# Performance work log

Hardware: AMD Instinct MI355X
Metric: run time of the kernel (lower is better)

The kernel has to match this reference:

```python
import jax, jax.numpy as jnp
import numpy as np

B, N, CZ, CH, CA, H, TN = 1, 256, 128, 128, 32, 4, 4


def setup_inputs() -> dict:
    key = jax.random.key(0)
    ks = iter(jax.random.split(key, 64))

    def rn(shape, s=0.02):
        return jax.random.normal(next(ks), shape, dtype=jnp.float32) * s

    d = {"z": jax.random.normal(next(ks), (B, N, N, CZ), dtype=jnp.float32)}
    # Triangle multiplication params, stacked [2, ...]: idx 0 = outgoing, 1 = incoming
    d["tm_ln_in_w"] = jnp.ones((2, CZ)); d["tm_ln_in_b"] = jnp.zeros((2, CZ))
    for nm, shp in [("ap", (2, CZ, CH)), ("ag", (2, CZ, CH)), ("bp", (2, CZ, CH)),
                    ("bg", (2, CZ, CH)), ("g", (2, CZ, CZ)), ("zo", (2, CH, CZ))]:
        d[f"tm_{nm}_w"] = rn(shp)
        d[f"tm_{nm}_b"] = jnp.zeros((2, shp[-1]))
    d["tm_lnout_w"] = jnp.ones((2, CH)); d["tm_lnout_b"] = jnp.zeros((2, CH))
    # Triangle attention params, stacked [2, ...]: idx 0 = start, 1 = end
    d["ta_ln_w"] = jnp.ones((2, CZ)); d["ta_ln_b"] = jnp.zeros((2, CZ))
    d["ta_q_w"] = rn((2, CZ, H * CA)); d["ta_k_w"] = rn((2, CZ, H * CA)); d["ta_v_w"] = rn((2, CZ, H * CA))
    d["ta_b_w"] = rn((2, CZ, H))
    d["ta_g_w"] = rn((2, CZ, H * CA)); d["ta_g_b"] = jnp.zeros((2, H * CA))
    d["ta_o_w"] = rn((2, H * CA, CZ)); d["ta_o_b"] = jnp.zeros((2, CZ))
    # Pair transition
    d["pt_ln_w"] = jnp.ones((CZ,)); d["pt_ln_b"] = jnp.zeros((CZ,))
    d["pt_1_w"] = rn((CZ, TN * CZ)); d["pt_1_b"] = jnp.zeros((TN * CZ,))
    d["pt_2_w"] = rn((TN * CZ, CZ)); d["pt_2_b"] = jnp.zeros((CZ,))
    return d


def _ln(x, w, b, eps=1e-5):
    m = jnp.mean(x, axis=-1, keepdims=True)
    v = jnp.mean(jnp.square(x - m), axis=-1, keepdims=True)
    return (x - m) * jax.lax.rsqrt(v + eps) * w + b


def _tri_mul(z, lnw, lnb, apw, apb, agw, agb, bpw, bpb, bgw, bgb, gw, gb,
             lnow, lnob, zw, zb, outgoing):
    x = _ln(z, lnw, lnb)
    a = jax.nn.sigmoid(x @ agw + agb) * (x @ apw + apb)  # [B,I,J,CH]
    b = jax.nn.sigmoid(x @ bgw + bgb) * (x @ bpw + bpb)
    eq = 'bikc,bjkc->bijc' if outgoing else 'bkic,bkjc->bijc'
    t = jnp.einsum(eq, a, b)  # O(N^3 * CH)
    t = _ln(t, lnow, lnob) @ zw + zb
    return t * jax.nn.sigmoid(x @ gw + gb)


def _tri_att(z, lnw, lnb, qw, kw, vw, bw, gw, gb, ow, ob):
    Bz, I, J, _ = z.shape
    x = _ln(z, lnw, lnb)
    # triangle bias [B,1,H,I,J] (broadcast over query row)
    bias = jnp.einsum('bijc,ch->bhij', x, bw)[:, None]
    q = (x @ qw).reshape(Bz, I, J, H, CA).transpose(0, 1, 3, 2, 4) / np.float32(np.sqrt(CA))
    k = (x @ kw).reshape(Bz, I, J, H, CA).transpose(0, 1, 3, 2, 4)
    v = (x @ vw).reshape(Bz, I, J, H, CA).transpose(0, 1, 3, 2, 4)
    a = jnp.einsum('bihqc,bihkc->bihqk', q, k) + bias  # [B,I,H,J,J]
    p = jax.nn.softmax(a, axis=-1)
    o = jnp.einsum('bihqk,bihkc->bihqc', p, v).transpose(0, 1, 3, 2, 4).reshape(Bz, I, J, H * CA)
    o = o * jax.nn.sigmoid(x @ gw + gb)
    return o @ ow + ob


def reference(z, tm_ln_in_w, tm_ln_in_b, tm_ap_w, tm_ap_b, tm_ag_w, tm_ag_b,
              tm_bp_w, tm_bp_b, tm_bg_w, tm_bg_b, tm_g_w, tm_g_b,
              tm_lnout_w, tm_lnout_b, tm_zo_w, tm_zo_b,
              ta_ln_w, ta_ln_b, ta_q_w, ta_k_w, ta_v_w, ta_b_w,
              ta_g_w, ta_g_b, ta_o_w, ta_o_b,
              pt_ln_w, pt_ln_b, pt_1_w, pt_1_b, pt_2_w, pt_2_b):
    def tm(zz, i, outgoing):
        return _tri_mul(zz, tm_ln_in_w[i], tm_ln_in_b[i], tm_ap_w[i], tm_ap_b[i],
                        tm_ag_w[i], tm_ag_b[i], tm_bp_w[i], tm_bp_b[i],
                        tm_bg_w[i], tm_bg_b[i], tm_g_w[i], tm_g_b[i],
                        tm_lnout_w[i], tm_lnout_b[i], tm_zo_w[i], tm_zo_b[i], outgoing)

    def ta(zz, i):
        return _tri_att(zz, ta_ln_w[i], ta_ln_b[i], ta_q_w[i], ta_k_w[i], ta_v_w[i],
                        ta_b_w[i], ta_g_w[i], ta_g_b[i], ta_o_w[i], ta_o_b[i])

    z = z + tm(z, 0, True)          # triangle mult outgoing + residual (dropout = eval identity)
    z = z + tm(z, 1, False)         # triangle mult incoming + residual
    z = z + ta(z, 0)                # triangle attention (starting node)
    zt = jnp.swapaxes(z, 1, 2)      # transpose for ending-node attention
    zt = zt + ta(zt, 1)
    z = jnp.swapaxes(zt, 1, 2)
    x = _ln(z, pt_ln_w, pt_ln_b)    # pair transition
    z = z + (jax.nn.relu(x @ pt_1_w + pt_1_b) @ pt_2_w + pt_2_b)
    return z
```

## Files before the change

### kernel.cpp

```cpp
#include <hip/hip_runtime.h>
#include <math.h>

#define N_  256
#define NN  65536
#define CZ  128
#define CH  128
#define H_  4
#define CA  32

typedef __attribute__((ext_vector_type(8))) short bf16x8;
typedef __attribute__((ext_vector_type(4))) float f32x4;

__device__ __forceinline__ float sigmoidf_(float x){ return 1.f/(1.f+__expf(-x)); }

__device__ __forceinline__ short f2b(float f){
  unsigned u = __float_as_uint(f);
  unsigned r = (u + 0x7fffu + ((u>>16)&1u)) >> 16;
  return (short)r;
}
__device__ __forceinline__ float b2f(short s){
  unsigned u = ((unsigned)(unsigned short)s) << 16;
  return __uint_as_float(u);
}
__device__ __forceinline__ unsigned pk_bf16(float lo, float hi){
  unsigned r;
  asm volatile("v_cvt_pk_bf16_f32 %0, %1, %2" : "=v"(r) : "v"(lo), "v"(hi));
  return r;
}

__device__ __forceinline__ void glds16(const void* g, const void* l){
  __builtin_amdgcn_global_load_lds((const __attribute__((address_space(1))) void*)g,
                                   (__attribute__((address_space(3))) void*)l, 16, 0, 0);
}

__device__ __forceinline__ float wave_red_sum(float v){
  #pragma unroll
  for(int o=32;o>0;o>>=1) v += __shfl_xor(v,o,64);
  return v;
}

__device__ __forceinline__ int Gperm(int t, int m){
  return ((t>>1)<<5) + ((m>>2)<<3) + ((t&1)<<2) + (m&3);
}

__global__ void __launch_bounds__(256) prep_weights(
    const float* tm_ag, const float* tm_ap, const float* tm_bg, const float* tm_bp,
    const float* tm_g, const float* tm_zo,
    const float* ta_q, const float* ta_k, const float* ta_v, const float* ta_g, const float* ta_o,
    const float* pt1, const float* pt2, short* Wf){
  int tid = threadIdx.x;
  int g = blockIdx.x*4 + (tid>>6);
  int l = tid & 63;
  int s = blockIdx.y;
  const float* src; int ldn = 128, koff = 0, noff = 0;
  if (s < 12){
    int i = s/6, w = s - i*6;
    switch(w){ case 0: src=tm_ag; break; case 1: src=tm_ap; break; case 2: src=tm_bg; break;
               case 3: src=tm_bp; break; case 4: src=tm_g;  break; default: src=tm_zo; }
    src += i*16384;
  } else if (s < 22){
    int t2 = s-12; int i = t2/5, w = t2 - i*5;
    switch(w){ case 0: src=ta_q; break; case 1: src=ta_k; break; case 2: src=ta_v; break;
               case 3: src=ta_g; break; default: src=ta_o; }
    src += i*16384;
  } else if (s < 26){
    src = pt1; ldn = 512; noff = (s-22)*128;
  } else {
    src = pt2; koff = (s-26)*128;
  }
  int nt = g>>2, ks = g&3;
  int n = noff + nt*16 + (l&15);
  int kb = koff + ks*32 + (l>>4)*8;
  short tmp[8];
  #pragma unroll
  for (int e=0;e<8;e++) tmp[e] = f2b(src[(size_t)(kb+e)*ldn + n]);
  short* dst = Wf + s*16384 + ((nt*4+ks)*64 + l)*8;
  *(short4*)dst     = *(short4*)&tmp[0];
  *(short4*)(dst+4) = *(short4*)&tmp[4];
}

template<bool TRANS>
__global__ void __launch_bounds__(256) ln_x(const float* __restrict__ in,
                                            const float* __restrict__ w,
                                            const float* __restrict__ b,
                                            short* __restrict__ out){
  int wid  = threadIdx.x >> 6;
  int lane = threadIdx.x & 63;
  int row  = blockIdx.x*4 + wid;
  int irow;
  if (TRANS){ int i = row >> 8, j = row & 255; irow = (j<<8) | i; } else irow = row;
  float v0 = in[(size_t)irow*CZ + lane];
  float v1 = in[(size_t)irow*CZ + lane + 64];
  float m  = wave_red_sum(v0+v1) * (1.f/128.f);
  float d0 = v0-m, d1 = v1-m;
  float var = wave_red_sum(d0*d0 + d1*d1) * (1.f/128.f);
  float r = rsqrtf(var + 1e-5f);
  out[(size_t)row*CZ + lane]      = f2b(d0*r*w[lane]    + b[lane]);
  out[(size_t)row*CZ + lane + 64] = f2b(d1*r*w[lane+64] + b[lane+64]);
}

__device__ __forceinline__ void stage128_8(const short* __restrict__ g, short* xs, int r0, int tid){
  #pragma unroll
  for (int m=0;m<4;++m){
    int d = m*512 + tid;
    int row = d>>4, cw = d&15;
    glds16(&g[(size_t)(r0+row)*128 + ((cw ^ (row&15))<<3)], xs + (size_t)(d & ~63)*8);
  }
}

__device__ __forceinline__ bf16x8 ldsA(const short* xs, int row, int ch){
  return *(const bf16x8*)&xs[row*128 + ((ch ^ (row&15))<<3)];
}

__device__ __forceinline__ void stageW(const short* __restrict__ wf, int h, short* wb, int tid){
  #pragma unroll
  for (int r=0;r<2;++r){
    int s = r*512 + tid;
    int ch = s>>6, ln = s&63;
    glds16(wf + (size_t)(((ch>>1)*4 + h*2 + (ch&1))*64 + ln)*8, wb + (size_t)(s & ~63)*8);
  }
}

__device__ __forceinline__ void core_half(const short* xs, const short* wb, int h,
                                          int wm, int wn, int l, f32x4 (&acc)[2][4]){
  #pragma unroll
  for (int ks2=0; ks2<2; ++ks2){
    bf16x8 a[2], b[4];
    #pragma unroll
    for (int mt=0; mt<2; ++mt)
      a[mt] = ldsA(xs, wm*32 + mt*16 + (l&15), (h*2+ks2)*4 + (l>>4));
    #pragma unroll
    for (int nt=0; nt<4; ++nt)
      b[nt] = *(const bf16x8*)&wb[(size_t)(((wn*4+nt)*2 + ks2)*64 + l)*8];
    #pragma unroll
    for (int mt=0; mt<2; ++mt)
      #pragma unroll
      for (int nt=0; nt<4; ++nt)
        acc[mt][nt] = __builtin_amdgcn_mfma_f32_16x16x32_bf16(a[mt], b[nt], acc[mt][nt], 0,0,0);
  }
}

#define ZERO_ACC(A) { _Pragma("unroll") for(int _a=0;_a<2;_a++) _Pragma("unroll") for(int _b=0;_b<4;_b++) A[_a][_b]=(f32x4){0,0,0,0}; }

#define GEMM_PROLOG8 \
  int tid = threadIdx.x; int r0 = blockIdx.x*128; \
  int wid = tid>>6, l = tid&63; int wm = wid>>1, wn = wid&1; (void)r0;

#define EPI8 \
  int row = wm*32 + mt*16 + ((l>>4)<<2) + reg; \
  int col = wn*64 + nt*16 + (l&15);

#define FOR_EPI for (int mt=0;mt<2;++mt) for (int nt=0;nt<4;++nt) for (int reg=0;reg<4;++reg)

#define SCATTER_PACKED(P, LDSBUF) \
  _Pragma("unroll") \
  for (int mt=0;mt<2;++mt) \
    _Pragma("unroll") \
    for (int nt=0;nt<4;++nt){ \
      int row0 = wm*32 + mt*16 + ((l>>4)<<2); \
      int col  = wn*64 + nt*16 + (l&15); \
      unsigned lo = (unsigned)P[mt][nt].x, hi = (unsigned)P[mt][nt].y; \
      LDSBUF[(row0  )*128 + (((col>>3) ^ ((row0  )&15))<<3) + (col&7)] = (short)(lo & 0xffff); \
      LDSBUF[(row0+1)*128 + (((col>>3) ^ ((row0+1)&15))<<3) + (col&7)] = (short)(lo >> 16); \
      LDSBUF[(row0+2)*128 + (((col>>3) ^ ((row0+2)&15))<<3) + (col&7)] = (short)(hi & 0xffff); \
      LDSBUF[(row0+3)*128 + (((col>>3) ^ ((row0+3)&15))<<3) + (col&7)] = (short)(hi >> 16); \
    }

#define STORE_TILE(OUT, LDSBUF) \
  _Pragma("unroll") \
  for (int m2=0;m2<4;++m2){ \
    int d = m2*512 + tid; int row = d>>4, ch = d&15; \
    *(int4*)&OUT[(size_t)(r0+row)*128 + ch*8] = *(const int4*)&LDSBUF[row*128 + ((ch ^ (row&15))<<3)]; \
  }

__global__ void __launch_bounds__(512,4) k_quad_gate(const short* __restrict__ X,
                                                     const short* __restrict__ Wagf, const float* __restrict__ bag,
                                                     const short* __restrict__ Wapf, const float* __restrict__ bap,
                                                     const short* __restrict__ Wbgf, const float* __restrict__ bbg,
                                                     const short* __restrict__ Wbpf, const float* __restrict__ bbp,
                                                     short* __restrict__ out1, short* __restrict__ out2){
  __shared__ short xs[16384];
  __shared__ short wb[2][8192];
  short* wbf = &wb[0][0];
  GEMM_PROLOG8
  stageW(Wagf, 0, wb[0], tid);
  stage128_8(X, xs, r0, tid);
  __syncthreads();
  int2 o1[2][4], o2[2][4];
  {
    f32x4 ag[2][4], ap[2][4];
    ZERO_ACC(ag) ZERO_ACC(ap)
    stageW(Wagf, 1, wb[1], tid); core_half(xs, wb[0], 0, wm, wn, l, ag); __syncthreads();
    stageW(Wapf, 0, wb[0], tid); core_half(xs, wb[1], 1, wm, wn, l, ag); __syncthreads();
    stageW(Wapf, 1, wb[1], tid); core_half(xs, wb[0], 0, wm, wn, l, ap); __syncthreads();
    stageW(Wbgf, 0, wb[0], tid); core_half(xs, wb[1], 1, wm, wn, l, ap); __syncthreads();
    #pragma unroll
    for (int mt=0;mt<2;++mt)
      #pragma unroll
      for (int nt=0;nt<4;++nt){
        int col = wn*64 + nt*16 + (l&15);
        float bgc = bag[col], bpc = bap[col];
        float v0 = (ap[mt][nt][0]+bpc)*sigmoidf_(ag[mt][nt][0]+bgc);
        float v1 = (ap[mt][nt][1]+bpc)*sigmoidf_(ag[mt][nt][1]+bgc);
        float v2 = (ap[mt][nt][2]+bpc)*sigmoidf_(ag[mt][nt][2]+bgc);
        float v3 = (ap[mt][nt][3]+bpc)*sigmoidf_(ag[mt][nt][3]+bgc);
        o1[mt][nt].x = (int)pk_bf16(v0,v1);
        o1[mt][nt].y = (int)pk_bf16(v2,v3);
      }
  }
  {
    f32x4 bg2[2][4], bp2[2][4];
    ZERO_ACC(bg2) ZERO_ACC(bp2)
    stageW(Wbgf, 1, wb[1], tid); core_half(xs, wb[0], 0, wm, wn, l, bg2); __syncthreads();
    stageW(Wbpf, 0, wb[0], tid); core_half(xs, wb[1], 1, wm, wn, l, bg2); __syncthreads();
    stageW(Wbpf, 1, wb[1], tid); core_half(xs, wb[0], 0, wm, wn, l, bp2); __syncthreads();
    core_half(xs, wb[1], 1, wm, wn, l, bp2);
    #pragma unroll
    for (int mt=0;mt<2;++mt)
      #pragma unroll
      for (int nt=0;nt<4;++nt){
        int col = wn*64 + nt*16 + (l&15);
        float bgc = bbg[col], bpc = bbp[col];
        float v0 = (bp2[mt][nt][0]+bpc)*sigmoidf_(bg2[mt][nt][0]+bgc);
        float v1 = (bp2[mt][nt][1]+bpc)*sigmoidf_(bg2[mt][nt][1]+bgc);
        float v2 = (bp2[mt][nt][2]+bpc)*sigmoidf_(bg2[mt][nt][2]+bgc);
        float v3 = (bp2[mt][nt][3]+bpc)*sigmoidf_(bg2[mt][nt][3]+bgc);
        o2[mt][nt].x = (int)pk_bf16(v0,v1);
        o2[mt][nt].y = (int)pk_bf16(v2,v3);
      }
  }
  __syncthreads();
  SCATTER_PACKED(o1, wbf)
  __syncthreads();
  STORE_TILE(out1, wbf)
  __syncthreads();
  SCATTER_PACKED(o2, wbf)
  __syncthreads();
  STORE_TILE(out2, wbf)
}

__global__ void __launch_bounds__(512,4) k_qkv(const short* __restrict__ X,
                                               const short* __restrict__ Wqf, float sq,
                                               const short* __restrict__ Wkf,
                                               const short* __restrict__ Wvf,
                                               const float* __restrict__ bw,
                                               short* __restrict__ out_q, short* __restrict__ out_k,
                                               short* __restrict__ Vt, float* __restrict__ BSF){
  __shared__ short xs[16384];
  __shared__ short wb[2][8192];
  short* wbf = &wb[0][0];
  GEMM_PROLOG8
  stageW(Wqf, 0, wb[0], tid);
  stage128_8(X, xs, r0, tid);
  __syncthreads();
  int2 oq[2][4], ok[2][4];
  {
    f32x4 aq[2][4], ak[2][4];
    ZERO_ACC(aq) ZERO_ACC(ak)
    stageW(Wqf, 1, wb[1], tid); core_half(xs, wb[0], 0, wm, wn, l, aq); __syncthreads();
    stageW(Wkf, 0, wb[0], tid); core_half(xs, wb[1], 1, wm, wn, l, aq); __syncthreads();
    #pragma unroll
    for (int mt=0;mt<2;++mt)
      #pragma unroll
      for (int nt=0;nt<4;++nt){
        oq[mt][nt].x = (int)pk_bf16(aq[mt][nt][0]*sq, aq[mt][nt][1]*sq);
        oq[mt][nt].y = (int)pk_bf16(aq[mt][nt][2]*sq, aq[mt][nt][3]*sq);
      }
    stageW(Wkf, 1, wb[1], tid); core_half(xs, wb[0], 0, wm, wn, l, ak); __syncthreads();
    stageW(Wvf, 0, wb[0], tid); core_half(xs, wb[1], 1, wm, wn, l, ak); __syncthreads();
    #pragma unroll
    for (int mt=0;mt<2;++mt)
      #pragma unroll
      for (int nt=0;nt<4;++nt){
        ok[mt][nt].x = (int)pk_bf16(ak[mt][nt][0], ak[mt][nt][1]);
        ok[mt][nt].y = (int)pk_bf16(ak[mt][nt][2], ak[mt][nt][3]);
      }
  }
  f32x4 av[2][4];
  ZERO_ACC(av)
  stageW(Wvf, 1, wb[1], tid); core_half(xs, wb[0], 0, wm, wn, l, av); __syncthreads();
  core_half(xs, wb[1], 1, wm, wn, l, av);
  {
    int rl = tid & 127, hh = tid >> 7;
    float bacc = 0.f;
    #pragma unroll
    for (int ch=0; ch<16; ++ch){
      bf16x8 v = ldsA(xs, rl, ch);
      #pragma unroll
      for (int e=0;e<8;++e) bacc += b2f(v[e]) * bw[(ch*8+e)*H_ + hh];
    }
    int r = r0 + rl;
    int qq = r >> 8, j = r & 255;
    int t = ((j>>5)<<1) + ((j>>2)&1);
    int mm = (((j>>3)&3)<<2) + (j&3);
    int idx = (((hh*16 + (qq>>4))*16 + t) << 8) + (((mm>>2)*16 + (qq&15)) << 2) + (mm&3);
    BSF[idx] = bacc;
  }
  __syncthreads();
  #pragma unroll
  for (int mt=0;mt<2;++mt)
    #pragma unroll
    for (int nt=0;nt<4;++nt){
      int rb  = wm*32 + mt*16 + ((l>>4)<<2);
      int col = wn*64 + nt*16 + (l&15);
      short4 s4 = { f2b(av[mt][nt][0]), f2b(av[mt][nt][1]), f2b(av[mt][nt][2]), f2b(av[mt][nt][3]) };
      *(short4*)&xs[col*128 + (((rb>>3) ^ (col&15))<<3) + (rb&7)] = s4;
    }
  __syncthreads();
  int i = r0>>8, j0 = r0&255;
  #pragma unroll
  for (int m=0;m<4;++m){
    int d = m*512 + tid;
    int c = d>>4, ch = d&15;
    int4 val = *(const int4*)&xs[c*128 + ((ch ^ (c&15))<<3)];
    *(int4*)&Vt[(size_t)((i*4 + (c>>5))*32 + (c&31))*256 + j0 + ch*8] = val;
  }
  SCATTER_PACKED(oq, wbf)
  __syncthreads();
  STORE_TILE(out_q, wbf)
  __syncthreads();
  SCATTER_PACKED(ok, wbf)
  __syncthreads();
  STORE_TILE(out_k, wbf)
}

__global__ void __launch_bounds__(512,2) k_tri_finish(const short* __restrict__ Tb,
                                                      const short* __restrict__ X,
                                                      const short* __restrict__ Wzf, const float* __restrict__ bz,
                                                      const short* __restrict__ Wgf, const float* __restrict__ bg,
                                                      const float* __restrict__ lnw, const float* __restrict__ lnb,
                                                      const float* __restrict__ zin, float* __restrict__ zout){
  __shared__ short tt[16384];
  __shared__ short xs[16384];
  __shared__ short wb[2][8192];
  __shared__ float ps[512], pq[512];
  __shared__ float mu[128], iv[128];
  GEMM_PROLOG8
  stageW(Wzf, 0, wb[0], tid);
  stage128_8(X, xs, r0, tid);
  #pragma unroll
  for (int m=0;m<4;++m){
    int d = m*512 + tid;
    int c = d>>4, ch = d&15;
    glds16(&Tb[(size_t)c*65536 + r0 + ch*8], tt + (size_t)(d & ~63)*8);
  }
  __syncthreads();
  int rl = tid & 127, cq = tid >> 7;
  float vals[32]; float s = 0.f, q = 0.f;
  #pragma unroll
  for (int cc=0; cc<32; ++cc){
    float v = b2f(tt[(cq*32+cc)*128 + rl]);
    vals[cc] = v; s += v; q += v*v;
  }
  ps[cq*128 + rl] = s; pq[cq*128 + rl] = q;
  __syncthreads();
  if (tid < 128){
    float ss = ps[tid]+ps[128+tid]+ps[256+tid]+ps[384+tid];
    float qq = pq[tid]+pq[128+tid]+pq[256+tid]+pq[384+tid];
    float m = ss * (1.f/128.f);
    float var = qq * (1.f/128.f) - m*m;
    mu[tid] = m; iv[tid] = rsqrtf(var + 1e-5f);
  }
  __syncthreads();
  {
    float m = mu[rl], r = iv[rl];
    #pragma unroll
    for (int chq=0; chq<4; ++chq){
      short tmp[8];
      #pragma unroll
      for (int e=0;e<8;++e){
        int cc = chq*8 + e;
        int c = cq*32 + cc;
        tmp[e] = f2b((vals[cc]-m)*r*lnw[c] + lnb[c]);
      }
      int ch = cq*4 + chq;
      *(int4*)&tt[rl*128 + ((ch ^ (rl&15))<<3)] = *(int4*)tmp;
    }
  }
  __syncthreads();
  f32x4 az[2][4], ag[2][4];
  ZERO_ACC(az) ZERO_ACC(ag)
  stageW(Wzf, 1, wb[1], tid); core_half(tt, wb[0], 0, wm, wn, l, az); __syncthreads();
  stageW(Wgf, 0, wb[0], tid); core_half(tt, wb[1], 1, wm, wn, l, az); __syncthreads();
  stageW(Wgf, 1, wb[1], tid); core_half(xs, wb[0], 0, wm, wn, l, ag); __syncthreads();
  core_half(xs, wb[1], 1, wm, wn, l, ag);
  FOR_EPI{
    EPI8
    size_t idx = (size_t)(r0+row)*128 + col;
    float v = (az[mt][nt][reg] + bz[col]) * sigmoidf_(ag[mt][nt][reg] + bg[col]);
    zout[idx] = zin[idx] + v;
  }
}

template<bool TRANS>
__global__ void __launch_bounds__(512,2) k_attn_out(const short* __restrict__ O,
                                                    const short* __restrict__ X,
                                                    const short* __restrict__ Wgf, const float* __restrict__ bg,
                                                    const short* __restrict__ Wof, const float* __restrict__ bo,
                                                    float* __restrict__ z){
  __shared__ short xs[16384];
  __shared__ short os[16384];
  __shared__ short wb[2][8192];
  GEMM_PROLOG8
  stageW(Wgf, 0, wb[0], tid);
  stage128_8(X, xs, r0, tid);
  #pragma unroll
  for (int m=0;m<4;++m){
    int d = m*512 + tid;
    int row = d>>4, ch = d&15;
    glds16(&O[(size_t)(r0+row)*128 + ch*8], os + (size_t)(d & ~63)*8);
  }
  __syncthreads();
  f32x4 ag[2][4];
  ZERO_ACC(ag)
  stageW(Wgf, 1, wb[1], tid); core_half(xs, wb[0], 0, wm, wn, l, ag); __syncthreads();
  stageW(Wof, 0, wb[0], tid); core_half(xs, wb[1], 1, wm, wn, l, ag); __syncthreads();
  stageW(Wof, 1, wb[1], tid);
  FOR_EPI{
    EPI8
    float ov = b2f(os[row*128 + col]);
    float v = ov * sigmoidf_(ag[mt][nt][reg] + bg[col]);
    xs[row*128 + (((col>>3) ^ (row&15))<<3) + (col&7)] = f2b(v);
  }
  __syncthreads();
  f32x4 a2[2][4];
  ZERO_ACC(a2)
  core_half(xs, wb[0], 0, wm, wn, l, a2);
  core_half(xs, wb[1], 1, wm, wn, l, a2);
  FOR_EPI{
    EPI8
    int orow = r0+row;
    int zrow = TRANS ? (((orow&255)<<8) | (orow>>8)) : orow;
    z[(size_t)zrow*128 + col] += a2[mt][nt][reg] + bo[col];
  }
}

__global__ void __launch_bounds__(512,2) k_pt(const float* __restrict__ lnw, const float* __restrict__ lnb,
                                              const short* __restrict__ W1f, const float* __restrict__ b1,
                                              const short* __restrict__ W2f, const float* __restrict__ b2,
                                              float* __restrict__ z){
  __shared__ short xs[16384];
  __shared__ short hs[16384];
  __shared__ short wb[2][8192];
  __shared__ float ps[512], pq[512];
  __shared__ float mu[128], iv[128];
  GEMM_PROLOG8
  stageW(W1f, 0, wb[0], tid);
  int rl = tid & 127, cq = tid >> 7;
  float vals[32]; float s = 0.f, q = 0.f;
  {
    const float* zr = &z[(size_t)(r0+rl)*128 + cq*32];
    #pragma unroll
    for (int cc=0; cc<32; cc+=4){
      float4 v4 = *(const float4*)&zr[cc];
      vals[cc]=v4.x; vals[cc+1]=v4.y; vals[cc+2]=v4.z; vals[cc+3]=v4.w;
      s += v4.x+v4.y+v4.z+v4.w;
      q += v4.x*v4.x + v4.y*v4.y + v4.z*v4.z + v4.w*v4.w;
    }
  }
  ps[cq*128 + rl] = s; pq[cq*128 + rl] = q;
  __syncthreads();
  if (tid < 128){
    float ss = ps[tid]+ps[128+tid]+ps[256+tid]+ps[384+tid];
    float qq = pq[tid]+pq[128+tid]+pq[256+tid]+pq[384+tid];
    float m = ss * (1.f/128.f);
    float var = qq * (1.f/128.f) - m*m;
    mu[tid] = m; iv[tid] = rsqrtf(var + 1e-5f);
  }
  __syncthreads();
  {
    float m = mu[rl], r = iv[rl];
    #pragma unroll
    for (int chq=0; chq<4; ++chq){
      short tmp[8];
      #pragma unroll
      for (int e=0;e<8;++e){
        int cc = chq*8 + e;
        int c = cq*32 + cc;
        tmp[e] = f2b((vals[cc]-m)*r*lnw[c] + lnb[c]);
      }
      int ch = cq*4 + chq;
      *(int4*)&xs[rl*128 + ((ch ^ (rl&15))<<3)] = *(int4*)tmp;
    }
  }
  __syncthreads();
  f32x4 a2[2][4];
  ZERO_ACC(a2)
  for (int m=0;m<4;++m){
    f32x4 a1[2][4];
    ZERO_ACC(a1)
    stageW(W1f + m*16384, 1, wb[1], tid); core_half(xs, wb[0], 0, wm, wn, l, a1); __syncthreads();
    stageW(W2f + m*16384, 0, wb[0], tid); core_half(xs, wb[1], 1, wm, wn, l, a1); __syncthreads();
    stageW(W2f + m*16384, 1, wb[1], tid);
    FOR_EPI{
      EPI8
      float v = fmaxf(a1[mt][nt][reg] + b1[m*128 + col], 0.f);
      hs[row*128 + (((col>>3) ^ (row&15))<<3) + (col&7)] = f2b(v);
    }
    __syncthreads();
    core_half(hs, wb[0], 0, wm, wn, l, a2);
    __syncthreads();
    if (m<3) stageW(W1f + (m+1)*16384, 0, wb[0], tid);
    core_half(hs, wb[1], 1, wm, wn, l, a2);
    __syncthreads();
  }
  FOR_EPI{
    EPI8
    z[(size_t)(r0+row)*128 + col] += a2[mt][nt][reg] + b2[col];
  }
}

template<bool TR>
__global__ void __launch_bounds__(256) pack_cxy(const short* __restrict__ inA, const short* __restrict__ inB,
                                                short* __restrict__ outA, short* __restrict__ outB){
  __shared__ short tile[256*144];
  const short* in = blockIdx.y ? inB : inA;
  short* out      = blockIdx.y ? outB : outA;
  int x = blockIdx.x, tid = threadIdx.x;
  #pragma unroll
  for (int m=0;m<16;++m){
    int idx = m*256 + tid;
    int y = idx>>4, c0 = (idx&15)*8;
    int r = TR ? (y*256 + x) : (x*256 + y);
    *(int4*)&tile[y*144 + c0] = *(const int4*)&in[(size_t)r*128 + c0];
  }
  __syncthreads();
  int c = tid & 127, yh = tid >> 7;
  short* ob = out + (size_t)c*65536 + x*256 + yh*128;
  #pragma unroll
  for (int yc=0; yc<16; ++yc){
    short tmp[8];
    #pragma unroll
    for (int e=0;e<8;e++) tmp[e] = tile[(yh*128 + yc*8 + e)*144 + c];
    *(int4*)&ob[yc*8] = *(int4*)tmp;
  }
}

__global__ void __launch_bounds__(512,4) k_einsum(const short* __restrict__ Ab,
                                                  const short* __restrict__ Bb,
                                                  short* __restrict__ Tb){
  __shared__ short as[2][128*64];
  __shared__ short bs[2][128*64];
  int c = blockIdx.z;
  int i0 = blockIdx.x*128, j0 = blockIdx.y*128;
  const short* A = Ab + (size_t)c*65536;
  const short* B = Bb + (size_t)c*65536;
  int tid = threadIdx.x;
  int wid = tid>>6, l = tid&63; int wm = wid>>1, wn = wid&1;
  f32x4 acc[2][4];
  ZERO_ACC(acc)

  #define ESTAGE(buf, kt) { \
    _Pragma("unroll") \
    for (int m_=0;m_<2;++m_){ \
      int d_ = m_*512 + tid; \
      int row_ = d_>>3, cw_ = d_&7; \
      glds16(&A[(size_t)(i0+row_)*256 + (kt)*64 + ((cw_ ^ (row_&7))<<3)], &as[buf][(d_ & ~63)*8]); \
      glds16(&B[(size_t)(j0+row_)*256 + (kt)*64 + ((cw_ ^ (row_&7))<<3)], &bs[buf][(d_ & ~63)*8]); \
    } }

  ESTAGE(0, 0)
  __syncthreads();
  for (int kt=0; kt<4; ++kt){
    int cur = kt & 1;
    if (kt < 3) ESTAGE(cur^1, kt+1)
    #pragma unroll
    for (int ks=0; ks<2; ++ks){
// ... 83 lines not shown
      w4.x = pk_bf16(acc[2*jt  ][0], acc[2*jt  ][1]);
      w4.y = pk_bf16(acc[2*jt  ][2], acc[2*jt  ][3]);
      w4.z = pk_bf16(acc[2*jt+1][0], acc[2*jt+1][1]);
      w4.w = pk_bf16(acc[2*jt+1][2], acc[2*jt+1][3]);
      pf[jt] = *(bf16x8*)&w4;
    }
    #pragma unroll
    for (int ct=0; ct<2; ++ct){
      f32x4 oe = {0.f,0.f,0.f,0.f}, oo = {0.f,0.f,0.f,0.f};
      #pragma unroll
      for (int jt=0;jt<8;jt+=2){
        bf16x8 ve = *(const bf16x8*)&Vf[((ct*8 + jt  )*64 + l)*8];
        bf16x8 vo = *(const bf16x8*)&Vf[((ct*8 + jt+1)*64 + l)*8];
        oe = __builtin_amdgcn_mfma_f32_16x16x32_bf16(ve, pf[jt  ], oe, 0,0,0);
        oo = __builtin_amdgcn_mfma_f32_16x16x32_bf16(vo, pf[jt+1], oo, 0,0,0);
      }
      int q = sub*16 + ln;
      int c = ct*16 + lg*4;
      short4 ov = { f2b((oe[0]+oo[0])*iv), f2b((oe[1]+oo[1])*iv),
                    f2b((oe[2]+oo[2])*iv), f2b((oe[3]+oo[3])*iv) };
      *(short4*)&O[(size_t)(i*N_ + q)*CH + h*CA + c] = ov;
    }
  }
}

extern "C" void kernel_launch(void* const* d_in, const int* in_sizes, int n_in,
                              void* d_out, int out_size, void* d_ws, size_t ws_size,
                              hipStream_t stream) {
  const float* z_in      = (const float*)d_in[0];
  const float* tm_lnin_w = (const float*)d_in[1];
  const float* tm_lnin_b = (const float*)d_in[2];
  const float* tm_ap_w   = (const float*)d_in[3];
  const float* tm_ap_b   = (const float*)d_in[4];
  const float* tm_ag_w   = (const float*)d_in[5];
  const float* tm_ag_b   = (const float*)d_in[6];
  const float* tm_bp_w   = (const float*)d_in[7];
  const float* tm_bp_b   = (const float*)d_in[8];
  const float* tm_bg_w   = (const float*)d_in[9];
  const float* tm_bg_b   = (const float*)d_in[10];
  const float* tm_g_w    = (const float*)d_in[11];
  const float* tm_g_b    = (const float*)d_in[12];
  const float* tm_zo_w   = (const float*)d_in[13];
  const float* tm_zo_b   = (const float*)d_in[14];
  const float* tm_lno_w  = (const float*)d_in[15];
  const float* tm_lno_b  = (const float*)d_in[16];
  const float* ta_ln_w   = (const float*)d_in[17];
  const float* ta_ln_b   = (const float*)d_in[18];
  const float* ta_q_w    = (const float*)d_in[19];
  const float* ta_k_w    = (const float*)d_in[20];
  const float* ta_v_w    = (const float*)d_in[21];
  const float* ta_b_w    = (const float*)d_in[22];
  const float* ta_g_w    = (const float*)d_in[23];
  const float* ta_g_b    = (const float*)d_in[24];
  const float* ta_o_w    = (const float*)d_in[25];
  const float* ta_o_b    = (const float*)d_in[26];
  const float* pt_ln_w   = (const float*)d_in[27];
  const float* pt_ln_b   = (const float*)d_in[28];
  const float* pt_1_w    = (const float*)d_in[29];
  const float* pt_1_b    = (const float*)d_in[30];
  const float* pt_2_w    = (const float*)d_in[31];
  const float* pt_2_b    = (const float*)d_in[32];

  float* z  = (float*)d_out;
  char* base = (char*)d_ws;
  const size_t MB = 1u<<20;
  short* wf  = (short*)base;
  short* Xb  = (short*)(base + 1*MB);
  short* R1  = (short*)(base + 17*MB);
  short* R2  = (short*)(base + 33*MB);
  short* R3  = (short*)(base + 49*MB);
  short* R4  = (short*)(base + 65*MB);
  short* Tb  = (short*)(base + 81*MB);
  float* BSF = (float*)(base + 113*MB);

  #define SL(s) (wf + (size_t)(s)*16384)

  prep_weights<<<dim3(8,30), 256, 0, stream>>>(tm_ag_w, tm_ap_w, tm_bg_w, tm_bp_w,
                                               tm_g_w, tm_zo_w,
                                               ta_q_w, ta_k_w, ta_v_w, ta_g_w, ta_o_w,
                                               pt_1_w, pt_2_w, wf);

  for (int i=0;i<2;i++){
    const float* zsrc = (i==0) ? z_in : z;
    ln_x<false><<<NN/4, 256, 0, stream>>>(zsrc, tm_lnin_w+i*CZ, tm_lnin_b+i*CZ, Xb);
    k_quad_gate<<<NN/128, 512, 0, stream>>>(Xb, SL(i*6+0), tm_ag_b+i*CH, SL(i*6+1), tm_ap_b+i*CH,
                                            SL(i*6+2), tm_bg_b+i*CH, SL(i*6+3), tm_bp_b+i*CH,
                                            R1, R2);
    if (i==0) pack_cxy<false><<<dim3(256,2), 256, 0, stream>>>(R1, R2, R3, R4);
    else      pack_cxy<true ><<<dim3(256,2), 256, 0, stream>>>(R1, R2, R3, R4);
    k_einsum<<<dim3(2,2,128), 512, 0, stream>>>(R3, R4, Tb);
    k_tri_finish<<<NN/128, 512, 0, stream>>>(Tb, Xb, SL(i*6+5), tm_zo_b+i*CZ,
                                             SL(i*6+4), tm_g_b+i*CZ,
                                             tm_lno_w+i*CH, tm_lno_b+i*CH, zsrc, z);
  }

  for (int i=0;i<2;i++){
    if (i==0) ln_x<false><<<NN/4, 256, 0, stream>>>(z, ta_ln_w, ta_ln_b, Xb);
    else      ln_x<true ><<<NN/4, 256, 0, stream>>>(z, ta_ln_w+CZ, ta_ln_b+CZ, Xb);
    k_qkv<<<NN/128, 512, 0, stream>>>(Xb, SL(12+i*5+0), 0.17677669529663687f,
                                      SL(12+i*5+1), SL(12+i*5+2), ta_b_w+i*CZ*H_,
                                      R1, R2, R3, BSF);
    attn_mfma<<<dim3(N_,H_), 256, 0, stream>>>(R1, R2, R3, BSF, R4);
    if (i==0) k_attn_out<false><<<NN/128, 512, 0, stream>>>(R4, Xb, SL(12+i*5+3), ta_g_b+i*H_*CA,
                                                            SL(12+i*5+4), ta_o_b+i*CZ, z);
    else      k_attn_out<true ><<<NN/128, 512, 0, stream>>>(R4, Xb, SL(12+i*5+3), ta_g_b+i*H_*CA,
                                                            SL(12+i*5+4), ta_o_b+i*CZ, z);
  }

  k_pt<<<NN/128, 512, 0, stream>>>(pt_ln_w, pt_ln_b, SL(22), pt_1_b, SL(26), pt_2_b, z);
}
```

Before: 534.9 us.

## Fuse input layernorm into projection GEMMs and shrink row tiles to 64

Removes the standalone ln_x kernels by computing the layernorm inside k_gg and k_qkv, which write the normalized bf16 tile to Xb for later consumers. All row-tiled GEMM kernels go from 128-row/512-thread blocks to 64-row/256-thread blocks, doubling the grid and cutting LDS per block. This saves a separate launch and one fp32 read pass per layernorm. In exchange, weight tiles are staged twice as often relative to the work done, and the extra Xb store adds to the fused kernels.

Measured after the change: 516.1 us. 3.5% less time.

```diff
diff --git a/kernel.cpp b/kernel.cpp
--- a/kernel.cpp
+++ b/kernel.cpp
@@ -31,12 +31,6 @@
 __device__ __forceinline__ void glds16(const void* g, const void* l){
   __builtin_amdgcn_global_load_lds((const __attribute__((address_space(1))) void*)g,
                                    (__attribute__((address_space(3))) void*)l, 16, 0, 0);
-}
-
-__device__ __forceinline__ float wave_red_sum(float v){
-  #pragma unroll
-  for(int o=32;o>0;o>>=1) v += __shfl_xor(v,o,64);
-  return v;
 }
 
 __device__ __forceinline__ int Gperm(int t, int m){
@@ -79,30 +73,10 @@
   *(short4*)(dst+4) = *(short4*)&tmp[4];
 }
 
-template<bool TRANS>
-__global__ void __launch_bounds__(256) ln_x(const float* __restrict__ in,
-                                            const float* __restrict__ w,
-                                            const float* __restrict__ b,
-                                            short* __restrict__ out){
-  int wid  = threadIdx.x >> 6;
-  int lane = threadIdx.x & 63;
-  int row  = blockIdx.x*4 + wid;
-  int irow;
-  if (TRANS){ int i = row >> 8, j = row & 255; irow = (j<<8) | i; } else irow = row;
-  float v0 = in[(size_t)irow*CZ + lane];
-  float v1 = in[(size_t)irow*CZ + lane + 64];
-  float m  = wave_red_sum(v0+v1) * (1.f/128.f);
-  float d0 = v0-m, d1 = v1-m;
-  float var = wave_red_sum(d0*d0 + d1*d1) * (1.f/128.f);
-  float r = rsqrtf(var + 1e-5f);
-  out[(size_t)row*CZ + lane]      = f2b(d0*r*w[lane]    + b[lane]);
-  out[(size_t)row*CZ + lane + 64] = f2b(d1*r*w[lane+64] + b[lane+64]);
-}
-
-__device__ __forceinline__ void stage128_8(const short* __restrict__ g, short* xs, int r0, int tid){
+__device__ __forceinline__ void stage64(const short* __restrict__ g, short* xs, int r0, int tid){
   #pragma unroll
   for (int m=0;m<4;++m){
-    int d = m*512 + tid;
+    int d = m*256 + tid;
     int row = d>>4, cw = d&15;
     glds16(&g[(size_t)(r0+row)*128 + ((cw ^ (row&15))<<3)], xs + (size_t)(d & ~63)*8);
   }
@@ -114,8 +88,8 @@
 
 __device__ __forceinline__ void stageW(const short* __restrict__ wf, int h, short* wb, int tid){
   #pragma unroll
-  for (int r=0;r<2;++r){
-    int s = r*512 + tid;
+  for (int r=0;r<4;++r){
+    int s = r*256 + tid;
     int ch = s>>6, ln = s&63;
     glds16(wf + (size_t)(((ch>>1)*4 + h*2 + (ch&1))*64 + ln)*8, wb + (size_t)(s & ~63)*8);
   }
@@ -142,8 +116,8 @@
 
 #define ZERO_ACC(A) { _Pragma("unroll") for(int _a=0;_a<2;_a++) _Pragma("unroll") for(int _b=0;_b<4;_b++) A[_a][_b]=(f32x4){0,0,0,0}; }
 
-#define GEMM_PROLOG8 \
-  int tid = threadIdx.x; int r0 = blockIdx.x*128; \
+#define GEMM_PROLOG \
+  int tid = threadIdx.x; int r0 = blockIdx.x*64; \
   int wid = tid>>6, l = tid&63; int wm = wid>>1, wn = wid&1; (void)r0;
 
 #define EPI8 \
@@ -169,96 +143,141 @@
 #define STORE_TILE(OUT, LDSBUF) \
   _Pragma("unroll") \
   for (int m2=0;m2<4;++m2){ \
-    int d = m2*512 + tid; int row = d>>4, ch = d&15; \
+    int d = m2*256 + tid; int row = d>>4, ch = d&15; \
     *(int4*)&OUT[(size_t)(r0+row)*128 + ch*8] = *(const int4*)&LDSBUF[row*128 + ((ch ^ (row&15))<<3)]; \
   }
 
-__global__ void __launch_bounds__(512,4) k_quad_gate(const short* __restrict__ X,
-                                                     const short* __restrict__ Wagf, const float* __restrict__ bag,
-                                                     const short* __restrict__ Wapf, const float* __restrict__ bap,
-                                                     const short* __restrict__ Wbgf, const float* __restrict__ bbg,
-                                                     const short* __restrict__ Wbpf, const float* __restrict__ bbp,
-                                                     short* __restrict__ out1, short* __restrict__ out2){
-  __shared__ short xs[16384];
+template<bool TRANS>
+__device__ __forceinline__ void ln_prolog(const float* __restrict__ zsrc,
+                                          const float* __restrict__ lnw,
+                                          const float* __restrict__ lnb,
+                                          int r0, int tid, short* xs,
+                                          float* ps, float* pq, float* mu, float* iv){
+  int rl = tid & 63, cq = tid >> 6;
+  int r = r0 + rl;
+  int sr = TRANS ? (((r&255)<<8) | (r>>8)) : r;
+  float vals[32]; float s=0.f, q=0.f;
+  const float* zr = &zsrc[(size_t)sr*128 + cq*32];
+  #pragma unroll
+  for (int cc=0; cc<32; cc+=4){
+    float4 v4 = *(const float4*)&zr[cc];
+    vals[cc]=v4.x; vals[cc+1]=v4.y; vals[cc+2]=v4.z; vals[cc+3]=v4.w;
+    s += v4.x+v4.y+v4.z+v4.w;
+    q += v4.x*v4.x+v4.y*v4.y+v4.z*v4.z+v4.w*v4.w;
+  }
+  ps[cq*64+rl]=s; pq[cq*64+rl]=q;
+  __syncthreads();
+  if (tid < 64){
+    float ss = ps[tid]+ps[64+tid]+ps[128+tid]+ps[192+tid];
+    float qq = pq[tid]+pq[64+tid]+pq[128+tid]+pq[192+tid];
+    float m = ss*(1.f/128.f);
+    float var = qq*(1.f/128.f) - m*m;
+    mu[tid]=m; iv[tid]=rsqrtf(var+1e-5f);
+  }
+  __syncthreads();
+  float m = mu[rl], rv = iv[rl];
+  #pragma unroll
+  for (int chq=0; chq<4; ++chq){
+    short tmp[8];
+    #pragma unroll
+    for (int e=0;e<8;++e){
+      int cc = chq*8+e, c = cq*32+cc;
+      tmp[e] = f2b((vals[cc]-m)*rv*lnw[c] + lnb[c]);
+    }
+    int ch = cq*4 + chq;
+    *(int4*)&xs[rl*128 + ((ch ^ (rl&15))<<3)] = *(int4*)tmp;
+  }
+}
+
+__global__ void __launch_bounds__(256,4) k_gg(const float* __restrict__ zsrc,
+                                              const float* __restrict__ lnw, const float* __restrict__ lnb,
+                                              const short* __restrict__ Wagf, const float* __restrict__ bag,
+                                              const short* __restrict__ Wapf, const float* __restrict__ bap,
+                                              const short* __restrict__ Wbgf, const float* __restrict__ bbg,
+                                              const short* __restrict__ Wbpf, const float* __restrict__ bbp,
+                                              short* __restrict__ Xb,
+                                              short* __restrict__ out1, short* __restrict__ out2){
+  __shared__ short xs[8192];
   __shared__ short wb[2][8192];
-  short* wbf = &wb[0][0];
-  GEMM_PROLOG8
+  __shared__ float ps[256], pq[256], mu[64], iv[64];
+  GEMM_PROLOG
   stageW(Wagf, 0, wb[0], tid);
-  stage128_8(X, xs, r0, tid);
-  __syncthreads();
+  ln_prolog<false>(zsrc, lnw, lnb, r0, tid, xs, ps, pq, mu, iv);
+  __syncthreads();
+  STORE_TILE(Xb, xs)
   int2 o1[2][4], o2[2][4];
   {
-    f32x4 ag[2][4], ap[2][4];
-    ZERO_ACC(ag) ZERO_ACC(ap)
-    stageW(Wagf, 1, wb[1], tid); core_half(xs, wb[0], 0, wm, wn, l, ag); __syncthreads();
-    stageW(Wapf, 0, wb[0], tid); core_half(xs, wb[1], 1, wm, wn, l, ag); __syncthreads();
-    stageW(Wapf, 1, wb[1], tid); core_half(xs, wb[0], 0, wm, wn, l, ap); __syncthreads();
-    stageW(Wbgf, 0, wb[0], tid); core_half(xs, wb[1], 1, wm, wn, l, ap); __syncthreads();
+    f32x4 ag[2][4]; ZERO_ACC(ag)
+    stageW(Wagf,1,wb[1],tid); core_half(xs,wb[0],0,wm,wn,l,ag); __syncthreads();
+    stageW(Wapf,0,wb[0],tid); core_half(xs,wb[1],1,wm,wn,l,ag); __syncthreads();
+    f32x4 ap[2][4]; ZERO_ACC(ap)
+    stageW(Wapf,1,wb[1],tid); core_half(xs,wb[0],0,wm,wn,l,ap); __syncthreads();
+    stageW(Wbgf,0,wb[0],tid); core_half(xs,wb[1],1,wm,wn,l,ap); __syncthreads();
     #pragma unroll
     for (int mt=0;mt<2;++mt)
       #pragma unroll
       for (int nt=0;nt<4;++nt){
         int col = wn*64 + nt*16 + (l&15);
         float bgc = bag[col], bpc = bap[col];
-        float v0 = (ap[mt][nt][0]+bpc)*sigmoidf_(ag[mt][nt][0]+bgc);
-        float v1 = (ap[mt][nt][1]+bpc)*sigmoidf_(ag[mt][nt][1]+bgc);
-        float v2 = (ap[mt][nt][2]+bpc)*sigmoidf_(ag[mt][nt][2]+bgc);
-        float v3 = (ap[mt][nt][3]+bpc)*sigmoidf_(ag[mt][nt][3]+bgc);
-        o1[mt][nt].x = (int)pk_bf16(v0,v1);
-        o1[mt][nt].y = (int)pk_bf16(v2,v3);
+        o1[mt][nt].x = (int)pk_bf16((ap[mt][nt][0]+bpc)*sigmoidf_(ag[mt][nt][0]+bgc),
+                                    (ap[mt][nt][1]+bpc)*sigmoidf_(ag[mt][nt][1]+bgc));
+        o1[mt][nt].y = (int)pk_bf16((ap[mt][nt][2]+bpc)*sigmoidf_(ag[mt][nt][2]+bgc),
+                                    (ap[mt][nt][3]+bpc)*sigmoidf_(ag[mt][nt][3]+bgc));
       }
   }
   {
-    f32x4 bg2[2][4], bp2[2][4];
-    ZERO_ACC(bg2) ZERO_ACC(bp2)
-    stageW(Wbgf, 1, wb[1], tid); core_half(xs, wb[0], 0, wm, wn, l, bg2); __syncthreads();
-    stageW(Wbpf, 0, wb[0], tid); core_half(xs, wb[1], 1, wm, wn, l, bg2); __syncthreads();
-    stageW(Wbpf, 1, wb[1], tid); core_half(xs, wb[0], 0, wm, wn, l, bp2); __syncthreads();
-    core_half(xs, wb[1], 1, wm, wn, l, bp2);
+    f32x4 bg2[2][4]; ZERO_ACC(bg2)
+    stageW(Wbgf,1,wb[1],tid); core_half(xs,wb[0],0,wm,wn,l,bg2); __syncthreads();
+    stageW(Wbpf,0,wb[0],tid); core_half(xs,wb[1],1,wm,wn,l,bg2); __syncthreads();
+    f32x4 bp2[2][4]; ZERO_ACC(bp2)
+    stageW(Wbpf,1,wb[1],tid); core_half(xs,wb[0],0,wm,wn,l,bp2); __syncthreads();
+    core_half(xs,wb[1],1,wm,wn,l,bp2);
     #pragma unroll
     for (int mt=0;mt<2;++mt)
       #pragma unroll
       for (int nt=0;nt<4;++nt){
         int col = wn*64 + nt*16 + (l&15);
         float bgc = bbg[col], bpc = bbp[col];
-        float v0 = (bp2[mt][nt][0]+bpc)*sigmoidf_(bg2[mt][nt][0]+bgc);
-        float v1 = (bp2[mt][nt][1]+bpc)*sigmoidf_(bg2[mt][nt][1]+bgc);
-        float v2 = (bp2[mt][nt][2]+bpc)*sigmoidf_(bg2[mt][nt][2]+bgc);
-        float v3 = (bp2[mt][nt][3]+bpc)*sigmoidf_(bg2[mt][nt][3]+bgc);
-        o2[mt][nt].x = (int)pk_bf16(v0,v1);
-        o2[mt][nt].y = (int)pk_bf16(v2,v3);
+        o2[mt][nt].x = (int)pk_bf16((bp2[mt][nt][0]+bpc)*sigmoidf_(bg2[mt][nt][0]+bgc),
+                                    (bp2[mt][nt][1]+bpc)*sigmoidf_(bg2[mt][nt][1]+bgc));
+        o2[mt][nt].y = (int)pk_bf16((bp2[mt][nt][2]+bpc)*sigmoidf_(bg2[mt][nt][2]+bgc),
+                                    (bp2[mt][nt][3]+bpc)*sigmoidf_(bg2[mt][nt][3]+bgc));
       }
   }
   __syncthreads();
-  SCATTER_PACKED(o1, wbf)
-  __syncthreads();
-  STORE_TILE(out1, wbf)
-  __syncthreads();
-  SCATTER_PACKED(o2, wbf)
-  __syncthreads();
-  STORE_TILE(out2, wbf)
-}
-
-__global__ void __launch_bounds__(512,4) k_qkv(const short* __restrict__ X,
+  SCATTER_PACKED(o1, xs)
+  __syncthreads();
+  STORE_TILE(out1, xs)
+  __syncthreads();
+  SCATTER_PACKED(o2, xs)
+  __syncthreads();
+  STORE_TILE(out2, xs)
+}
+
+template<bool TRANS>
+__global__ void __launch_bounds__(256,4) k_qkv(const float* __restrict__ zsrc,
+                                               const float* __restrict__ lnw, const float* __restrict__ lnb,
                                                const short* __restrict__ Wqf, float sq,
                                                const short* __restrict__ Wkf,
                                                const short* __restrict__ Wvf,
                                                const float* __restrict__ bw,
+                                               short* __restrict__ Xb,
                                                short* __restrict__ out_q, short* __restrict__ out_k,
                                                short* __restrict__ Vt, float* __restrict__ BSF){
-  __shared__ short xs[16384];
+  __shared__ short xs[8192];
   __shared__ short wb[2][8192];
-  short* wbf = &wb[0][0];
-  GEMM_PROLOG8
+  __shared__ float ps[256], pq[256], mu[64], iv[64];
+  GEMM_PROLOG
   stageW(Wqf, 0, wb[0], tid);
-  stage128_8(X, xs, r0, tid);
-  __syncthreads();
+  ln_prolog<TRANS>(zsrc, lnw, lnb, r0, tid, xs, ps, pq, mu, iv);
+  __syncthreads();
+  STORE_TILE(Xb, xs)
   int2 oq[2][4], ok[2][4];
+  f32x4 av[2][4];
   {
-    f32x4 aq[2][4], ak[2][4];
-    ZERO_ACC(aq) ZERO_ACC(ak)
-    stageW(Wqf, 1, wb[1], tid); core_half(xs, wb[0], 0, wm, wn, l, aq); __syncthreads();
-    stageW(Wkf, 0, wb[0], tid); core_half(xs, wb[1], 1, wm, wn, l, aq); __syncthreads();
+    f32x4 aq[2][4]; ZERO_ACC(aq)
+    stageW(Wqf,1,wb[1],tid); core_half(xs,wb[0],0,wm,wn,l,aq); __syncthreads();
+    stageW(Wkf,0,wb[0],tid); core_half(xs,wb[1],1,wm,wn,l,aq); __syncthreads();
     #pragma unroll
     for (int mt=0;mt<2;++mt)
       #pragma unroll
@@ -266,8 +285,11 @@
         oq[mt][nt].x = (int)pk_bf16(aq[mt][nt][0]*sq, aq[mt][nt][1]*sq);
         oq[mt][nt].y = (int)pk_bf16(aq[mt][nt][2]*sq, aq[mt][nt][3]*sq);
       }
-    stageW(Wkf, 1, wb[1], tid); core_half(xs, wb[0], 0, wm, wn, l, ak); __syncthreads();
-    stageW(Wvf, 0, wb[0], tid); core_half(xs, wb[1], 1, wm, wn, l, ak); __syncthreads();
+  }
+  {
+    f32x4 ak[2][4]; ZERO_ACC(ak)
+    stageW(Wkf,1,wb[1],tid); core_half(xs,wb[0],0,wm,wn,l,ak); __syncthreads();
+    stageW(Wvf,0,wb[0],tid); core_half(xs,wb[1],1,wm,wn,l,ak); __syncthreads();
     #pragma unroll
     for (int mt=0;mt<2;++mt)
       #pragma unroll
@@ -276,12 +298,11 @@
         ok[mt][nt].y = (int)pk_bf16(ak[mt][nt][2], ak[mt][nt][3]);
       }
   }
-  f32x4 av[2][4];
   ZERO_ACC(av)
-  stageW(Wvf, 1, wb[1], tid); core_half(xs, wb[0], 0, wm, wn, l, av); __syncthreads();
-  core_half(xs, wb[1], 1, wm, wn, l, av);
+  stageW(Wvf,1,wb[1],tid); core_half(xs,wb[0],0,wm,wn,l,av); __syncthreads();
+  core_half(xs,wb[1],1,wm,wn,l,av);
   {
-    int rl = tid & 127, hh = tid >> 7;
+    int rl = tid & 63, hh = tid >> 6;
     float bacc = 0.f;
     #pragma unroll
     for (int ch=0; ch<16; ++ch){
@@ -304,66 +325,68 @@
       int rb  = wm*32 + mt*16 + ((l>>4)<<2);
       int col = wn*64 + nt*16 + (l&15);
       short4 s4 = { f2b(av[mt][nt][0]), f2b(av[mt][nt][1]), f2b(av[mt][nt][2]), f2b(av[mt][nt][3]) };
-      *(short4*)&xs[col*128 + (((rb>>3) ^ (col&15))<<3) + (rb&7)] = s4;
-    }
-  __syncthreads();
-  int i = r0>>8, j0 = r0&255;
-  #pragma unroll
-  for (int m=0;m<4;++m){
-    int d = m*512 + tid;
-    int c = d>>4, ch = d&15;
-    int4 val = *(const int4*)&xs[c*128 + ((ch ^ (c&15))<<3)];
-    *(int4*)&Vt[(size_t)((i*4 + (c>>5))*32 + (c&31))*256 + j0 + ch*8] = val;
-  }
-  SCATTER_PACKED(oq, wbf)
-  __syncthreads();
-  STORE_TILE(out_q, wbf)
-  __syncthreads();
-  SCATTER_PACKED(ok, wbf)
-  __syncthreads();
-  STORE_TILE(out_k, wbf)
-}
-
-__global__ void __launch_bounds__(512,2) k_tri_finish(const short* __restrict__ Tb,
+      *(short4*)&xs[col*64 + (((rb>>3) ^ (col&7))<<3) + (rb&7)] = s4;
+    }
+  __syncthreads();
+  {
+    int i = r0>>8, j0 = r0&255;
+    #pragma unroll
+    for (int m=0;m<4;++m){
+      int d = m*256 + tid;
+      int c = d>>3, jch = d&7;
+      int4 val = *(const int4*)&xs[c*64 + ((jch ^ (c&7))<<3)];
+      *(int4*)&Vt[(size_t)((i*4 + (c>>5))*32 + (c&31))*256 + j0 + jch*8] = val;
+    }
+  }
+  __syncthreads();
+  SCATTER_PACKED(oq, xs)
+  __syncthreads();
+  STORE_TILE(out_q, xs)
+  __syncthreads();
+  SCATTER_PACKED(ok, xs)
+  __syncthreads();
+  STORE_TILE(out_k, xs)
+}
+
+__global__ void __launch_bounds__(256,3) k_tri_finish(const short* __restrict__ Tb,
                                                       const short* __restrict__ X,
                                                       const short* __restrict__ Wzf, const float* __restrict__ bz,
                                                       const short* __restrict__ Wgf, const float* __restrict__ bg,
                                                       const float* __restrict__ lnw, const float* __restrict__ lnb,
                                                       const float* __restrict__ zin, float* __restrict__ zout){
-  __shared__ short tt[16384];
-  __shared__ short xs[16384];
+  __shared__ short tt[8192];
+  __shared__ short xs[8192];
   __shared__ short wb[2][8192];
-  __shared__ float ps[512], pq[512];
-  __shared__ float mu[128], iv[128];
-  GEMM_PROLOG8
+  __shared__ float ps[256], pq[256], mu[64], iv[64];
+  GEMM_PROLOG
   stageW(Wzf, 0, wb[0], tid);
-  stage128_8(X, xs, r0, tid);
+  stage64(X, xs, r0, tid);
   #pragma unroll
   for (int m=0;m<4;++m){
-    int d = m*512 + tid;
-    int c = d>>4, ch = d&15;
-    glds16(&Tb[(size_t)c*65536 + r0 + ch*8], tt + (size_t)(d & ~63)*8);
-  }
-  __syncthreads();
-  int rl = tid & 127, cq = tid >> 7;
+    int d = m*256 + tid;
+    int c = d>>3, jch = d&7;
+    glds16(&Tb[(size_t)c*65536 + r0 + jch*8], tt + (size_t)(d & ~63)*8);
+  }
+  __syncthreads();
+  int rl = tid & 63, cq = tid >> 6;
   float vals[32]; float s = 0.f, q = 0.f;
   #pragma unroll
   for (int cc=0; cc<32; ++cc){
-    float v = b2f(tt[(cq*32+cc)*128 + rl]);
+    float v = b2f(tt[(cq*32+cc)*64 + rl]);
     vals[cc] = v; s += v; q += v*v;
   }
-  ps[cq*128 + rl] = s; pq[cq*128 + rl] = q;
-  __syncthreads();
-  if (tid < 128){
-    float ss = ps[tid]+ps[128+tid]+ps[256+tid]+ps[384+tid];
-    float qq = pq[tid]+pq[128+tid]+pq[256+tid]+pq[384+tid];
+  ps[cq*64 + rl] = s; pq[cq*64 + rl] = q;
+  __syncthreads();
+  if (tid < 64){
+    float ss = ps[tid]+ps[64+tid]+ps[128+tid]+ps[192+tid];
+    float qq = pq[tid]+pq[64+tid]+pq[128+tid]+pq[192+tid];
     float m = ss * (1.f/128.f);
     float var = qq * (1.f/128.f) - m*m;
     mu[tid] = m; iv[tid] = rsqrtf(var + 1e-5f);
   }
   __syncthreads();
   {
-    float m = mu[rl], r = iv[rl];
+    float m = mu[rl], rv = iv[rl];
     #pragma unroll
     for (int chq=0; chq<4; ++chq){
       short tmp[8];
@@ -371,7 +394,7 @@
       for (int e=0;e<8;++e){
         int cc = chq*8 + e;
         int c = cq*32 + cc;
-        tmp[e] = f2b((vals[cc]-m)*r*lnw[c] + lnb[c]);
+        tmp[e] = f2b((vals[cc]-m)*rv*lnw[c] + lnb[c]);
       }
       int ch = cq*4 + chq;
       *(int4*)&tt[rl*128 + ((ch ^ (rl&15))<<3)] = *(int4*)tmp;
@@ -393,20 +416,20 @@
 }
 
 template<bool TRANS>
-__global__ void __launch_bounds__(512,2) k_attn_out(const short* __restrict__ O,
+__global__ void __launch_bounds__(256,3) k_attn_out(const short* __restrict__ O,
                                                     const short* __restrict__ X,
                                                     const short* __restrict__ Wgf, const float* __restrict__ bg,
                                                     const short* __restrict__ Wof, const float* __restrict__ bo,
                                                     float* __restrict__ z){
-  __shared__ short xs[16384];
-  __shared__ short os[16384];
+  __shared__ short xs[8192];
+  __shared__ short os[8192];
   __shared__ short wb[2][8192];
-  GEMM_PROLOG8
+  GEMM_PROLOG
   stageW(Wgf, 0, wb[0], tid);
-  stage128_8(X, xs, r0, tid);
+  stage64(X, xs, r0, tid);
   #pragma unroll
   for (int m=0;m<4;++m){
-    int d = m*512 + tid;
+    int d = m*256 + tid;
     int row = d>>4, ch = d&15;
     glds16(&O[(size_t)(r0+row)*128 + ch*8], os + (size_t)(d & ~63)*8);
   }
@@ -435,54 +458,17 @@
   }
 }
 
-__global__ void __launch_bounds__(512,2) k_pt(const float* __restrict__ lnw, const float* __restrict__ lnb,
+__global__ void __launch_bounds__(256,3) k_pt(const float* __restrict__ lnw, const float* __restrict__ lnb,
                                               const short* __restrict__ W1f, const float* __restrict__ b1,
                                               const short* __restrict__ W2f, const float* __restrict__ b2,
                                               float* __restrict__ z){
-  __shared__ short xs[16384];
-  __shared__ short hs[16384];
+  __shared__ short xs[8192];
+  __shared__ short hs[8192];
   __shared__ short wb[2][8192];
-  __shared__ float ps[512], pq[512];
-  __shared__ float mu[128], iv[128];
-  GEMM_PROLOG8
+  __shared__ float ps[256], pq[256], mu[64], iv[64];
+  GEMM_PROLOG
   stageW(W1f, 0, wb[0], tid);
-  int rl = tid & 127, cq = tid >> 7;
-  float vals[32]; float s = 0.f, q = 0.f;
-  {
-    const float* zr = &z[(size_t)(r0+rl)*128 + cq*32];
-    #pragma unroll
-    for (int cc=0; cc<32; cc+=4){
-      float4 v4 = *(const float4*)&zr[cc];
-      vals[cc]=v4.x; vals[cc+1]=v4.y; vals[cc+2]=v4.z; vals[cc+3]=v4.w;
-      s += v4.x+v4.y+v4.z+v4.w;
-      q += v4.x*v4.x + v4.y*v4.y + v4.z*v4.z + v4.w*v4.w;
-    }
-  }
-  ps[cq*128 + rl] = s; pq[cq*128 + rl] = q;
-  __syncthreads();
-  if (tid < 128){
-    float ss = ps[tid]+ps[128+tid]+ps[256+tid]+ps[384+tid];
-    float qq = pq[tid]+pq[128+tid]+pq[256+tid]+pq[384+tid];
-    float m = ss * (1.f/128.f);
-    float var = qq * (1.f/128.f) - m*m;
-    mu[tid] = m; iv[tid] = rsqrtf(var + 1e-5f);
-  }
-  __syncthreads();
-  {
-    float m = mu[rl], r = iv[rl];
-    #pragma unroll
-    for (int chq=0; chq<4; ++chq){
-      short tmp[8];
-      #pragma unroll
-      for (int e=0;e<8;++e){
-        int cc = chq*8 + e;
-        int c = cq*32 + cc;
-        tmp[e] = f2b((vals[cc]-m)*r*lnw[c] + lnb[c]);
-      }
-      int ch = cq*4 + chq;
-      *(int4*)&xs[rl*128 + ((ch ^ (rl&15))<<3)] = *(int4*)tmp;
-    }
-  }
+  ln_prolog<false>(z, lnw, lnb, r0, tid, xs, ps, pq, mu, iv);
   __syncthreads();
   f32x4 a2[2][4];
   ZERO_ACC(a2)
@@ -732,30 +718,33 @@
 
   for (int i=0;i<2;i++){
     const float* zsrc = (i==0) ? z_in : z;
-    ln_x<false><<<NN/4, 256, 0, stream>>>(zsrc, tm_lnin_w+i*CZ, tm_lnin_b+i*CZ, Xb);
-    k_quad_gate<<<NN/128, 512, 0, stream>>>(Xb, SL(i*6+0), tm_ag_b+i*CH, SL(i*6+1), tm_ap_b+i*CH,
-                                            SL(i*6+2), tm_bg_b+i*CH, SL(i*6+3), tm_bp_b+i*CH,
-                                            R1, R2);
+    k_gg<<<NN/64, 256, 0, stream>>>(zsrc, tm_lnin_w+i*CZ, tm_lnin_b+i*CZ,
+                                    SL(i*6+0), tm_ag_b+i*CH, SL(i*6+1), tm_ap_b+i*CH,
+                                    SL(i*6+2), tm_bg_b+i*CH, SL(i*6+3), tm_bp_b+i*CH,
+                                    Xb, R1, R2);
     if (i==0) pack_cxy<false><<<dim3(256,2), 256, 0, stream>>>(R1, R2, R3, R4);
     else      pack_cxy<true ><<<dim3(256,2), 256, 0, stream>>>(R1, R2, R3, R4);
     k_einsum<<<dim3(2,2,128), 512, 0, stream>>>(R3, R4, Tb);
-    k_tri_finish<<<NN/128, 512, 0, stream>>>(Tb, Xb, SL(i*6+5), tm_zo_b+i*CZ,
-                                             SL(i*6+4), tm_g_b+i*CZ,
-                                             tm_lno_w+i*CH, tm_lno_b+i*CH, zsrc, z);
+    k_tri_finish<<<NN/64, 256, 0, stream>>>(Tb, Xb, SL(i*6+5), tm_zo_b+i*CZ,
+                                            SL(i*6+4), tm_g_b+i*CZ,
+                                            tm_lno_w+i*CH, tm_lno_b+i*CH, zsrc, z);
   }
 
   for (int i=0;i<2;i++){
-    if (i==0) ln_x<false><<<NN/4, 256, 0, stream>>>(z, ta_ln_w, ta_ln_b, Xb);
-    else      ln_x<true ><<<NN/4, 256, 0, stream>>>(z, ta_ln_w+CZ, ta_ln_b+CZ, Xb);
-    k_qkv<<<NN/128, 512, 0, stream>>>(Xb, SL(12+i*5+0), 0.17677669529663687f,
-                                      SL(12+i*5+1), SL(12+i*5+2), ta_b_w+i*CZ*H_,
-                                      R1, R2, R3, BSF);
+    if (i==0)
+      k_qkv<false><<<NN/64, 256, 0, stream>>>(z, ta_ln_w, ta_ln_b,
+                                              SL(12+0), 0.17677669529663687f, SL(12+1), SL(12+2),
+                                              ta_b_w, Xb, R1, R2, R3, BSF);
+    else
+      k_qkv<true ><<<NN/64, 256, 0, stream>>>(z, ta_ln_w+CZ, ta_ln_b+CZ,
+                                              SL(17+0), 0.17677669529663687f, SL(17+1), SL(17+2),
+                                              ta_b_w+CZ*H_, Xb, R1, R2, R3, BSF);
     attn_mfma<<<dim3(N_,H_), 256, 0, stream>>>(R1, R2, R3, BSF, R4);
-    if (i==0) k_attn_out<false><<<NN/128, 512, 0, stream>>>(R4, Xb, SL(12+i*5+3), ta_g_b+i*H_*CA,
-                                                            SL(12+i*5+4), ta_o_b+i*CZ, z);
-    else      k_attn_out<true ><<<NN/128, 512, 0, stream>>>(R4, Xb, SL(12+i*5+3), ta_g_b+i*H_*CA,
-                                                            SL(12+i*5+4), ta_o_b+i*CZ, z);
-  }
-
-  k_pt<<<NN/128, 512, 0, stream>>>(pt_ln_w, pt_ln_b, SL(22), pt_1_b, SL(26), pt_2_b, z);
-}
+    if (i==0) k_attn_out<false><<<NN/64, 256, 0, stream>>>(R4, Xb, SL(12+3), ta_g_b,
+                                                           SL(12+4), ta_o_b, z);
+    else      k_attn_out<true ><<<NN/64, 256, 0, stream>>>(R4, Xb, SL(17+3), ta_g_b+H_*CA,
+                                                           SL(17+4), ta_o_b+CZ, z);
+  }
+
+  k_pt<<<NN/64, 256, 0, stream>>>(pt_ln_w, pt_ln_b, SL(22), pt_1_b, SL(26), pt_2_b, z);
+}
```
